# Kernel optimization log

Measured on AMD Instinct MI355X. Metric: run time of the kernel, lower is better.

The kernel has to match this reference:

```python
import jax, jax.numpy as jnp
import numpy as np

# Grid derived from voxel_size=[0.2,0.2,0.2], pcr=[0,-40,-3,70.4,40,1]
NX, NY, NZ, NB = 352, 400, 20, 4


def setup_inputs() -> dict:
    key = jax.random.key(0)
    N, C = 1_000_000, 64
    kp, kb, kz, ky, kx = jax.random.split(key, 5)
    points = jax.random.normal(kp, (N, C), dtype=jnp.float32)
    b = jax.random.randint(kb, (N,), 0, NB)
    z = jax.random.randint(kz, (N,), 0, NZ)
    y = jax.random.randint(ky, (N,), 0, NY)
    x = jax.random.randint(kx, (N,), 0, NX)
    coors = jnp.stack([b, z, y, x], axis=1).astype(jnp.int32)
    return {"points": points, "coors": coors}


def reference(points, coors):
    # Dynamic scatter with mean reduction (average_points=True):
    # group points sharing the same (batch, z, y, x) voxel coordinate and
    # average their features. Padded (unused) voxel slots have coor == -1
    # and zero features, so the output shape is static ([N, C]).
    N = points.shape[0]
    b, z, y, x = coors[:, 0], coors[:, 1], coors[:, 2], coors[:, 3]
    keys = ((b.astype(jnp.int64) * NZ + z) * NY + y) * NX + x  # linearized voxel id

    uniq, inv = jnp.unique(keys, return_inverse=True, size=N, fill_value=-1)
    inv = inv.reshape(-1)

    sums = jax.ops.segment_sum(points, inv, num_segments=N)          # [N, C]
    counts = jax.ops.segment_sum(jnp.ones((N,), points.dtype), inv, num_segments=N)
    voxels = sums / jnp.maximum(counts, 1.0)[:, None]

    # decode linearized keys back to (batch, z, y, x); -1 marks padding
    valid = uniq >= 0
    ux = uniq % NX
    uy = (uniq // NX) % NY
    uz = (uniq // (NX * NY)) % NZ
    ub = uniq // (NX * NY * NZ)
    voxel_coors = jnp.stack([ub, uz, uy, ux], axis=1).astype(jnp.int32)
    voxel_coors = jnp.where(valid[:, None], voxel_coors, -1)
    return voxels, voxel_coors
```

## Files before the change

kernel.cpp:

```cpp
#include <hip/hip_runtime.h>
#include <stdint.h>

#define NXc 352
#define NYc 400
#define NZc 20
#define KS  11264000
#define WORDS 176000
#define NBLKS 688
#define NCH 64
#define RPT 4

#define OFF_A     0ull
#define OFF_P     11264000ull
#define OFF_R     12672000ull
#define OFF_M     13376000ull
#define OFF_BP    14784000ull
#define OFF_BC    14788096ull
#define OFF_BM    14792192ull
#define OFF_NU    14796288ull
#define OFF_KEYPT 14796544ull
#define OFF_IOFF  18796544ull
#define OFF_ML    22796800ull
#define OFF_PID   24796800ull

static __device__ __forceinline__ int keyof(int4 c) {
  return ((c.x * NZc + c.y) * NYc + c.z) * NXc + c.w;
}

__global__ void k_zero(uint4* __restrict__ A4, unsigned int mA) {
  unsigned int i = blockIdx.x * 256 + threadIdx.x, s = gridDim.x * 256;
  uint4 z = make_uint4(0u, 0u, 0u, 0u);
  for (unsigned int j = i; j < mA; j += s) A4[j] = z;
}

__global__ void k_count(const int4* __restrict__ coors, unsigned int* __restrict__ A32,
                        int* __restrict__ keyPt, int n) {
  int p = blockIdx.x * 256 + threadIdx.x;
  if (p >= n) return;
  int key = keyof(coors[p]);
  keyPt[p] = key;
  atomicAdd(&A32[key >> 2], 1u << (8 * (key & 3)));
}

__global__ void k_scan1(const unsigned char* __restrict__ A, unsigned int* __restrict__ bp,
                        unsigned int* __restrict__ bc, unsigned int* __restrict__ bm) {
  int b = blockIdx.x, t = threadIdx.x;
  int w = b * 256 + t;
  unsigned int pres = 0, cnt = 0, mult = 0;
  if (w < WORDS) {
    const uint4* aw = (const uint4*)(A + (size_t)w * 64);
    unsigned long long mask = 0ull;
#pragma unroll
    for (int q = 0; q < 4; q++) {
      uint4 v = aw[q];
      unsigned int us[4] = { v.x, v.y, v.z, v.w };
#pragma unroll
      for (int i = 0; i < 4; i++) {
        unsigned int u = us[i];
#pragma unroll
        for (int bb = 0; bb < 4; bb++) {
          unsigned int byte = (u >> (8 * bb)) & 0xFFu;
          cnt += byte;
          mult += (byte >= 2u);
          if (byte) mask |= 1ull << (q * 16 + i * 4 + bb);
        }
      }
    }
    pres = (unsigned int)__popcll(mask);
  }
  __shared__ unsigned int sp[256], sc[256], sm[256];
  sp[t] = pres; sc[t] = cnt; sm[t] = mult; __syncthreads();
  for (int o = 128; o > 0; o >>= 1) {
    if (t < o) { sp[t] += sp[t + o]; sc[t] += sc[t + o]; sm[t] += sm[t + o]; }
    __syncthreads();
  }
  if (t == 0) { bp[b] = sp[0]; bc[b] = sc[0]; bm[b] = sm[0]; }
}

__global__ void k_scan2(unsigned int* __restrict__ bp, unsigned int* __restrict__ bc,
                        unsigned int* __restrict__ bm, unsigned int* __restrict__ nu,
                        unsigned int* __restrict__ ioff, int n) {
  int t = threadIdx.x;
  __shared__ unsigned int sp[256], sc[256], sm[256];
  unsigned int cp = 0, cc = 0, cm = 0;
  for (int base = 0; base < NBLKS; base += 256) {
    int i = base + t;
    unsigned int vp = (i < NBLKS) ? bp[i] : 0u;
    unsigned int vc = (i < NBLKS) ? bc[i] : 0u;
    unsigned int vm = (i < NBLKS) ? bm[i] : 0u;
    sp[t] = vp; sc[t] = vc; sm[t] = vm; __syncthreads();
    unsigned int ipv = vp, icv = vc, imv = vm;
    for (int o = 1; o < 256; o <<= 1) {
      unsigned int ap = (t >= o) ? sp[t - o] : 0u;
      unsigned int ac = (t >= o) ? sc[t - o] : 0u;
      unsigned int am = (t >= o) ? sm[t - o] : 0u;
      __syncthreads();
      ipv += ap; icv += ac; imv += am;
      sp[t] = ipv; sc[t] = icv; sm[t] = imv; __syncthreads();
    }
    if (i < NBLKS) { bp[i] = cp + ipv - vp; bc[i] = cc + icv - vc; bm[i] = cm + imv - vm; }
    unsigned int tp = sp[255], tc = sc[255], tm = sm[255];
    __syncthreads();
    cp += tp; cc += tc; cm += tm;
  }
  if (t == 0) { nu[0] = cp; nu[1] = cm; ioff[cp] = (unsigned int)n; }
}

__global__ void k_scan3(const unsigned char* __restrict__ A,
                        const unsigned int* __restrict__ bp, const unsigned int* __restrict__ bc,
                        const unsigned int* __restrict__ bm,
                        unsigned long long* __restrict__ P, unsigned int* __restrict__ R,
                        unsigned long long* __restrict__ M,
                        unsigned int* __restrict__ ioff, unsigned int* __restrict__ mlist,
                        float4* __restrict__ outc) {
  int b = blockIdx.x, t = threadIdx.x;
  int w = b * 256 + t;
  unsigned long long mask = 0ull, mmask = 0ull;
  unsigned int uu[16];
  unsigned int pres = 0, cnt = 0, mult = 0;
  if (w < WORDS) {
    const uint4* aw = (const uint4*)(A + (size_t)w * 64);
#pragma unroll
    for (int q = 0; q < 4; q++) {
      uint4 v = aw[q];
      uu[q * 4 + 0] = v.x; uu[q * 4 + 1] = v.y; uu[q * 4 + 2] = v.z; uu[q * 4 + 3] = v.w;
    }
#pragma unroll
    for (int i = 0; i < 16; i++) {
      unsigned int u = uu[i];
#pragma unroll
      for (int bb = 0; bb < 4; bb++) {
        unsigned int byte = (u >> (8 * bb)) & 0xFFu;
        cnt += byte;
        mult += (byte >= 2u);
        if (byte)       mask  |= 1ull << (i * 4 + bb);
        if (byte >= 2u) mmask |= 1ull << (i * 4 + bb);
      }
    }
    pres = (unsigned int)__popcll(mask);
  }
  __shared__ unsigned int sp[256], sc[256], sm[256];
  sp[t] = pres; sc[t] = cnt; sm[t] = mult; __syncthreads();
  unsigned int ip = pres, ic = cnt, im = mult;
  for (int o = 1; o < 256; o <<= 1) {
    unsigned int ap = (t >= o) ? sp[t - o] : 0u;
    unsigned int ac = (t >= o) ? sc[t - o] : 0u;
    unsigned int am = (t >= o) ? sm[t - o] : 0u;
    __syncthreads();
    ip += ap; ic += ac; im += am;
    sp[t] = ip; sc[t] = ic; sm[t] = im; __syncthreads();
  }
  if (w < WORDS) {
    unsigned int rank  = bp[b] + ip - pres;
    unsigned int coff  = bc[b] + ic - cnt;
    unsigned int mrank = bm[b] + im - mult;
    P[w] = mask; R[w] = rank; M[w] = mmask;
    for (int j = 0; j < 64; j++) {
      unsigned int byte = (uu[j >> 2] >> (8 * (j & 3))) & 0xFFu;
      if (byte) {
        ioff[rank] = coff;
        unsigned int k = (unsigned int)w * 64u + (unsigned int)j;
        unsigned int x = k % NXc; unsigned int k2 = k / NXc;
        unsigned int y = k2 % NYc; unsigned int k3 = k2 / NYc;
        unsigned int z = k3 % NZc; unsigned int bb2 = k3 / NZc;
        outc[rank] = make_float4((float)bb2, (float)z, (float)y, (float)x);
        if (byte >= 2u) mlist[mrank++] = rank;
        rank++; coff += byte;
      }
    }
  }
}

__global__ void k_scatter(const float4* __restrict__ pts, const int* __restrict__ keyPt,
                          unsigned int* __restrict__ A32,
                          const unsigned long long* __restrict__ P, const unsigned int* __restrict__ R,
                          const unsigned long long* __restrict__ M,
                          const unsigned int* __restrict__ ioff, unsigned int* __restrict__ pid,
                          float* __restrict__ out, int n) {
  int gt = blockIdx.x * 256 + threadIdx.x;
  int grp = gt >> 4, l = gt & 15;
  int pb = grp * RPT;
  if (pb >= n) return;
  int np = min(RPT, n - pb);

  float4 v[RPT];
#pragma unroll
  for (int j = 0; j < RPT; j++) {
    int p = pb + ((j < np) ? j : 0);
    v[j] = pts[(size_t)p * 16 + l];
  }
  int key[RPT];
#pragma unroll
  for (int j = 0; j < RPT; j++) key[j] = keyPt[pb + ((j < np) ? j : 0)];

  unsigned long long Pw[RPT], Mw[RPT];
  unsigned int Rw[RPT];
#pragma unroll
  for (int j = 0; j < RPT; j++) {
    int w = key[j] >> 6;
    Pw[j] = P[w]; Mw[j] = M[w]; Rw[j] = R[w];
  }

#pragma unroll
  for (int j = 0; j < RPT; j++) {
    if (j >= np) break;
    int bit = key[j] & 63;
    unsigned int rank = Rw[j] + (unsigned int)__popcll(Pw[j] & ((1ull << bit) - 1ull));
    if (!((Mw[j] >> bit) & 1ull)) {
      ((float4*)out)[(size_t)rank * 16 + l] = v[j];
    } else if (l == 0) {
      unsigned int sh = 8u * (unsigned int)(key[j] & 3);
      unsigned int old = atomicSub(&A32[key[j] >> 2], 1u << sh);
      unsigned int intra = ((old >> sh) & 0xFFu) - 1u;
      pid[ioff[rank] + intra] = (unsigned int)(pb + j);
    }
  }
}

__global__ void k_fin(const float4* __restrict__ pts, const unsigned int* __restrict__ pid,
                      const unsigned int* __restrict__ ioff, const unsigned int* __restrict__ mlist,
                      const unsigned int* __restrict__ nu, float* __restrict__ out, int n) {
  unsigned int s = gridDim.x * 256;
  unsigned int tid = blockIdx.x * 256 + threadIdx.x;
  unsigned int mc16 = nu[1] * 16u;
  for (unsigned int gt = tid; gt < mc16; gt += s) {
    unsigned int g = gt >> 4, l = gt & 15;
    unsigned int rank = mlist[g];
    unsigned int o0 = ioff[rank], o1 = ioff[rank + 1];
    float4 acc = make_float4(0.f, 0.f, 0.f, 0.f);
    for (unsigned int i = o0; i < o1; i++) {
      float4 v = pts[(size_t)pid[i] * 16 + l];
      acc.x += v.x; acc.y += v.y; acc.z += v.z; acc.w += v.w;
    }
    float inv = 1.0f / (float)(o1 - o0);
    acc.x *= inv; acc.y *= inv; acc.z *= inv; acc.w *= inv;
    ((float4*)out)[(size_t)rank * 16 + l] = acc;
  }
  unsigned int nU = nu[0];
  float4 z = make_float4(0.f, 0.f, 0.f, 0.f);
  float4 m1 = make_float4(-1.f, -1.f, -1.f, -1.f);
  for (unsigned int r = nU + tid; r < (unsigned int)n; r += s) {
    float4* row = (float4*)out + (size_t)r * 16;
#pragma unroll
    for (int q = 0; q < 16; q++) row[q] = z;
    ((float4*)(out + (size_t)n * NCH))[r] = m1;
  }
}

extern "C" void kernel_launch(void* const* d_in, const int* in_sizes, int n_in,
                              void* d_out, int out_size, void* d_ws, size_t ws_size,
                              hipStream_t stream) {
  const float4* pts = (const float4*)d_in[0];
  const int4* coors = (const int4*)d_in[1];
  int n = in_sizes[1] / 4;
  float* out = (float*)d_out;
  char* ws = (char*)d_ws;
  unsigned char*      A    = (unsigned char*)(ws + OFF_A);
  unsigned int*       A32  = (unsigned int*)(ws + OFF_A);
  unsigned long long* P    = (unsigned long long*)(ws + OFF_P);
  unsigned int*       R    = (unsigned int*)(ws + OFF_R);
  unsigned long long* M    = (unsigned long long*)(ws + OFF_M);
  unsigned int*       bp   = (unsigned int*)(ws + OFF_BP);
  unsigned int*       bc   = (unsigned int*)(ws + OFF_BC);
  unsigned int*       bm   = (unsigned int*)(ws + OFF_BM);
  unsigned int*       nu   = (unsigned int*)(ws + OFF_NU);
  int*                keyPt= (int*)(ws + OFF_KEYPT);
  unsigned int*       ioff = (unsigned int*)(ws + OFF_IOFF);
  unsigned int*       mlist= (unsigned int*)(ws + OFF_ML);
  unsigned int*       pid  = (unsigned int*)(ws + OFF_PID);
  float4*             outc = (float4*)(out + (size_t)n * NCH);

  k_zero   <<<2048,  256, 0, stream>>>((uint4*)A, (unsigned int)(KS / 16));
  int nb = (n + 255) / 256;
  k_count  <<<nb,    256, 0, stream>>>(coors, A32, keyPt, n);
  k_scan1  <<<NBLKS, 256, 0, stream>>>(A, bp, bc, bm);
  k_scan2  <<<1,     256, 0, stream>>>(bp, bc, bm, nu, ioff, n);
  k_scan3  <<<NBLKS, 256, 0, stream>>>(A, bp, bc, bm, P, R, M, ioff, mlist, outc);
  int ngrp = (n + RPT - 1) / RPT;
  int sb = (ngrp * 16 + 255) / 256;
  k_scatter<<<sb,    256, 0, stream>>>(pts, keyPt, A32, P, R, M, ioff, pid, out, n);
  k_fin    <<<2048,  256, 0, stream>>>(pts, pid, ioff, mlist, nu, out, n);
}
```

Measured before the change: 209.2 us.

## Replace multi-point voxel gather with pre-zeroed float atomic accumulation

The point-ID bucketing path for voxels with multiple points is removed, along with the per-voxel offset/count scans, the multi-mask, the mlist, and the gather in the final kernel. Rows for multi-point voxels are now zeroed during the compaction scan. The scatter kernel then atomically adds each point's features pre-scaled by 1/count, with the count read directly from the byte histogram. This drops a kernel phase and two of the three scan streams, but adds float atomics and makes summation order nondeterministic.

```diff
diff --git a/kernel.cpp b/kernel.cpp
--- a/kernel.cpp
+++ b/kernel.cpp
@@ -13,15 +13,9 @@
 #define OFF_A     0ull
 #define OFF_P     11264000ull
 #define OFF_R     12672000ull
-#define OFF_M     13376000ull
-#define OFF_BP    14784000ull
-#define OFF_BC    14788096ull
-#define OFF_BM    14792192ull
-#define OFF_NU    14796288ull
-#define OFF_KEYPT 14796544ull
-#define OFF_IOFF  18796544ull
-#define OFF_ML    22796800ull
-#define OFF_PID   24796800ull
+#define OFF_BP    13376000ull
+#define OFF_NU    13380096ull
+#define OFF_KEYPT 13380352ull
 
 static __device__ __forceinline__ int keyof(int4 c) {
   return ((c.x * NZc + c.y) * NYc + c.z) * NXc + c.w;
@@ -42,11 +36,10 @@
   atomicAdd(&A32[key >> 2], 1u << (8 * (key & 3)));
 }
 
-__global__ void k_scan1(const unsigned char* __restrict__ A, unsigned int* __restrict__ bp,
-                        unsigned int* __restrict__ bc, unsigned int* __restrict__ bm) {
+__global__ void k_scan1(const unsigned char* __restrict__ A, unsigned int* __restrict__ bp) {
   int b = blockIdx.x, t = threadIdx.x;
   int w = b * 256 + t;
-  unsigned int pres = 0, cnt = 0, mult = 0;
+  unsigned int pres = 0;
   if (w < WORDS) {
     const uint4* aw = (const uint4*)(A + (size_t)w * 64);
     unsigned long long mask = 0ull;
@@ -58,66 +51,52 @@
       for (int i = 0; i < 4; i++) {
         unsigned int u = us[i];
 #pragma unroll
-        for (int bb = 0; bb < 4; bb++) {
-          unsigned int byte = (u >> (8 * bb)) & 0xFFu;
-          cnt += byte;
-          mult += (byte >= 2u);
-          if (byte) mask |= 1ull << (q * 16 + i * 4 + bb);
-        }
+        for (int bb = 0; bb < 4; bb++)
+          if ((u >> (8 * bb)) & 0xFFu) mask |= 1ull << (q * 16 + i * 4 + bb);
       }
     }
     pres = (unsigned int)__popcll(mask);
   }
-  __shared__ unsigned int sp[256], sc[256], sm[256];
-  sp[t] = pres; sc[t] = cnt; sm[t] = mult; __syncthreads();
+  __shared__ unsigned int sp[256];
+  sp[t] = pres; __syncthreads();
   for (int o = 128; o > 0; o >>= 1) {
-    if (t < o) { sp[t] += sp[t + o]; sc[t] += sc[t + o]; sm[t] += sm[t + o]; }
+    if (t < o) sp[t] += sp[t + o];
     __syncthreads();
   }
-  if (t == 0) { bp[b] = sp[0]; bc[b] = sc[0]; bm[b] = sm[0]; }
-}
-
-__global__ void k_scan2(unsigned int* __restrict__ bp, unsigned int* __restrict__ bc,
-                        unsigned int* __restrict__ bm, unsigned int* __restrict__ nu,
-                        unsigned int* __restrict__ ioff, int n) {
+  if (t == 0) bp[b] = sp[0];
+}
+
+__global__ void k_scan2(unsigned int* __restrict__ bp, unsigned int* __restrict__ nu) {
   int t = threadIdx.x;
-  __shared__ unsigned int sp[256], sc[256], sm[256];
-  unsigned int cp = 0, cc = 0, cm = 0;
+  __shared__ unsigned int sp[256];
+  unsigned int cp = 0;
   for (int base = 0; base < NBLKS; base += 256) {
     int i = base + t;
     unsigned int vp = (i < NBLKS) ? bp[i] : 0u;
-    unsigned int vc = (i < NBLKS) ? bc[i] : 0u;
-    unsigned int vm = (i < NBLKS) ? bm[i] : 0u;
-    sp[t] = vp; sc[t] = vc; sm[t] = vm; __syncthreads();
-    unsigned int ipv = vp, icv = vc, imv = vm;
+    sp[t] = vp; __syncthreads();
+    unsigned int ipv = vp;
     for (int o = 1; o < 256; o <<= 1) {
       unsigned int ap = (t >= o) ? sp[t - o] : 0u;
-      unsigned int ac = (t >= o) ? sc[t - o] : 0u;
-      unsigned int am = (t >= o) ? sm[t - o] : 0u;
       __syncthreads();
-      ipv += ap; icv += ac; imv += am;
-      sp[t] = ipv; sc[t] = icv; sm[t] = imv; __syncthreads();
-    }
-    if (i < NBLKS) { bp[i] = cp + ipv - vp; bc[i] = cc + icv - vc; bm[i] = cm + imv - vm; }
-    unsigned int tp = sp[255], tc = sc[255], tm = sm[255];
+      ipv += ap;
+      sp[t] = ipv; __syncthreads();
+    }
+    if (i < NBLKS) bp[i] = cp + ipv - vp;
+    unsigned int tp = sp[255];
     __syncthreads();
-    cp += tp; cc += tc; cm += tm;
-  }
-  if (t == 0) { nu[0] = cp; nu[1] = cm; ioff[cp] = (unsigned int)n; }
-}
-
-__global__ void k_scan3(const unsigned char* __restrict__ A,
-                        const unsigned int* __restrict__ bp, const unsigned int* __restrict__ bc,
-                        const unsigned int* __restrict__ bm,
+    cp += tp;
+  }
+  if (t == 0) nu[0] = cp;
+}
+
+__global__ void k_scan3(const unsigned char* __restrict__ A, const unsigned int* __restrict__ bp,
                         unsigned long long* __restrict__ P, unsigned int* __restrict__ R,
-                        unsigned long long* __restrict__ M,
-                        unsigned int* __restrict__ ioff, unsigned int* __restrict__ mlist,
-                        float4* __restrict__ outc) {
+                        float4* __restrict__ outc, float* __restrict__ out) {
   int b = blockIdx.x, t = threadIdx.x;
   int w = b * 256 + t;
-  unsigned long long mask = 0ull, mmask = 0ull;
+  unsigned long long mask = 0ull;
   unsigned int uu[16];
-  unsigned int pres = 0, cnt = 0, mult = 0;
+  unsigned int pres = 0;
   if (w < WORDS) {
     const uint4* aw = (const uint4*)(A + (size_t)w * 64);
 #pragma unroll
@@ -129,53 +108,46 @@
     for (int i = 0; i < 16; i++) {
       unsigned int u = uu[i];
 #pragma unroll
-      for (int bb = 0; bb < 4; bb++) {
-        unsigned int byte = (u >> (8 * bb)) & 0xFFu;
-        cnt += byte;
-        mult += (byte >= 2u);
-        if (byte)       mask  |= 1ull << (i * 4 + bb);
-        if (byte >= 2u) mmask |= 1ull << (i * 4 + bb);
-      }
+      for (int bb = 0; bb < 4; bb++)
+        if ((u >> (8 * bb)) & 0xFFu) mask |= 1ull << (i * 4 + bb);
     }
     pres = (unsigned int)__popcll(mask);
   }
-  __shared__ unsigned int sp[256], sc[256], sm[256];
-  sp[t] = pres; sc[t] = cnt; sm[t] = mult; __syncthreads();
-  unsigned int ip = pres, ic = cnt, im = mult;
+  __shared__ unsigned int sp[256];
+  sp[t] = pres; __syncthreads();
+  unsigned int ip = pres;
   for (int o = 1; o < 256; o <<= 1) {
     unsigned int ap = (t >= o) ? sp[t - o] : 0u;
-    unsigned int ac = (t >= o) ? sc[t - o] : 0u;
-    unsigned int am = (t >= o) ? sm[t - o] : 0u;
     __syncthreads();
-    ip += ap; ic += ac; im += am;
-    sp[t] = ip; sc[t] = ic; sm[t] = im; __syncthreads();
+    ip += ap;
+    sp[t] = ip; __syncthreads();
   }
   if (w < WORDS) {
-    unsigned int rank  = bp[b] + ip - pres;
-    unsigned int coff  = bc[b] + ic - cnt;
-    unsigned int mrank = bm[b] + im - mult;
-    P[w] = mask; R[w] = rank; M[w] = mmask;
+    unsigned int rank = bp[b] + ip - pres;
+    P[w] = mask; R[w] = rank;
+    float4 z4 = make_float4(0.f, 0.f, 0.f, 0.f);
     for (int j = 0; j < 64; j++) {
       unsigned int byte = (uu[j >> 2] >> (8 * (j & 3))) & 0xFFu;
       if (byte) {
-        ioff[rank] = coff;
         unsigned int k = (unsigned int)w * 64u + (unsigned int)j;
         unsigned int x = k % NXc; unsigned int k2 = k / NXc;
         unsigned int y = k2 % NYc; unsigned int k3 = k2 / NYc;
         unsigned int z = k3 % NZc; unsigned int bb2 = k3 / NZc;
         outc[rank] = make_float4((float)bb2, (float)z, (float)y, (float)x);
-        if (byte >= 2u) mlist[mrank++] = rank;
-        rank++; coff += byte;
+        if (byte >= 2u) {
+          float4* row = (float4*)out + (size_t)rank * 16;
+#pragma unroll
+          for (int q = 0; q < 16; q++) row[q] = z4;
+        }
+        rank++;
       }
     }
   }
 }
 
 __global__ void k_scatter(const float4* __restrict__ pts, const int* __restrict__ keyPt,
-                          unsigned int* __restrict__ A32,
+                          const unsigned char* __restrict__ A,
                           const unsigned long long* __restrict__ P, const unsigned int* __restrict__ R,
-                          const unsigned long long* __restrict__ M,
-                          const unsigned int* __restrict__ ioff, unsigned int* __restrict__ pid,
                           float* __restrict__ out, int n) {
   int gt = blockIdx.x * 256 + threadIdx.x;
   int grp = gt >> 4, l = gt & 15;
@@ -193,12 +165,12 @@
 #pragma unroll
   for (int j = 0; j < RPT; j++) key[j] = keyPt[pb + ((j < np) ? j : 0)];
 
-  unsigned long long Pw[RPT], Mw[RPT];
-  unsigned int Rw[RPT];
+  unsigned long long Pw[RPT];
+  unsigned int Rw[RPT], cnt[RPT];
 #pragma unroll
   for (int j = 0; j < RPT; j++) {
     int w = key[j] >> 6;
-    Pw[j] = P[w]; Mw[j] = M[w]; Rw[j] = R[w];
+    Pw[j] = P[w]; Rw[j] = R[w]; cnt[j] = A[key[j]];
   }
 
 #pragma unroll
@@ -206,40 +178,25 @@
     if (j >= np) break;
     int bit = key[j] & 63;
     unsigned int rank = Rw[j] + (unsigned int)__popcll(Pw[j] & ((1ull << bit) - 1ull));
-    if (!((Mw[j] >> bit) & 1ull)) {
+    if (cnt[j] == 1u) {
       ((float4*)out)[(size_t)rank * 16 + l] = v[j];
-    } else if (l == 0) {
-      unsigned int sh = 8u * (unsigned int)(key[j] & 3);
-      unsigned int old = atomicSub(&A32[key[j] >> 2], 1u << sh);
-      unsigned int intra = ((old >> sh) & 0xFFu) - 1u;
-      pid[ioff[rank] + intra] = (unsigned int)(pb + j);
-    }
-  }
-}
-
-__global__ void k_fin(const float4* __restrict__ pts, const unsigned int* __restrict__ pid,
-                      const unsigned int* __restrict__ ioff, const unsigned int* __restrict__ mlist,
-                      const unsigned int* __restrict__ nu, float* __restrict__ out, int n) {
+    } else {
+      float inv = 1.0f / (float)cnt[j];
+      float* dst = out + (size_t)rank * 64 + l * 4;
+      atomicAdd(dst + 0, v[j].x * inv);
+      atomicAdd(dst + 1, v[j].y * inv);
+      atomicAdd(dst + 2, v[j].z * inv);
+      atomicAdd(dst + 3, v[j].w * inv);
+    }
+  }
+}
+
+__global__ void k_tail(const unsigned int* __restrict__ nu, float* __restrict__ out, int n) {
+  unsigned int nU = nu[0];
   unsigned int s = gridDim.x * 256;
-  unsigned int tid = blockIdx.x * 256 + threadIdx.x;
-  unsigned int mc16 = nu[1] * 16u;
-  for (unsigned int gt = tid; gt < mc16; gt += s) {
-    unsigned int g = gt >> 4, l = gt & 15;
-    unsigned int rank = mlist[g];
-    unsigned int o0 = ioff[rank], o1 = ioff[rank + 1];
-    float4 acc = make_float4(0.f, 0.f, 0.f, 0.f);
-    for (unsigned int i = o0; i < o1; i++) {
-      float4 v = pts[(size_t)pid[i] * 16 + l];
-      acc.x += v.x; acc.y += v.y; acc.z += v.z; acc.w += v.w;
-    }
-    float inv = 1.0f / (float)(o1 - o0);
-    acc.x *= inv; acc.y *= inv; acc.z *= inv; acc.w *= inv;
-    ((float4*)out)[(size_t)rank * 16 + l] = acc;
-  }
-  unsigned int nU = nu[0];
   float4 z = make_float4(0.f, 0.f, 0.f, 0.f);
   float4 m1 = make_float4(-1.f, -1.f, -1.f, -1.f);
-  for (unsigned int r = nU + tid; r < (unsigned int)n; r += s) {
+  for (unsigned int r = nU + blockIdx.x * 256 + threadIdx.x; r < (unsigned int)n; r += s) {
     float4* row = (float4*)out + (size_t)r * 16;
 #pragma unroll
     for (int q = 0; q < 16; q++) row[q] = z;
@@ -259,25 +216,19 @@
   unsigned int*       A32  = (unsigned int*)(ws + OFF_A);
   unsigned long long* P    = (unsigned long long*)(ws + OFF_P);
   unsigned int*       R    = (unsigned int*)(ws + OFF_R);
-  unsigned long long* M    = (unsigned long long*)(ws + OFF_M);
   unsigned int*       bp   = (unsigned int*)(ws + OFF_BP);
-  unsigned int*       bc   = (unsigned int*)(ws + OFF_BC);
-  unsigned int*       bm   = (unsigned int*)(ws + OFF_BM);
   unsigned int*       nu   = (unsigned int*)(ws + OFF_NU);
   int*                keyPt= (int*)(ws + OFF_KEYPT);
-  unsigned int*       ioff = (unsigned int*)(ws + OFF_IOFF);
-  unsigned int*       mlist= (unsigned int*)(ws + OFF_ML);
-  unsigned int*       pid  = (unsigned int*)(ws + OFF_PID);
   float4*             outc = (float4*)(out + (size_t)n * NCH);
 
   k_zero   <<<2048,  256, 0, stream>>>((uint4*)A, (unsigned int)(KS / 16));
   int nb = (n + 255) / 256;
   k_count  <<<nb,    256, 0, stream>>>(coors, A32, keyPt, n);
-  k_scan1  <<<NBLKS, 256, 0, stream>>>(A, bp, bc, bm);
-  k_scan2  <<<1,     256, 0, stream>>>(bp, bc, bm, nu, ioff, n);
-  k_scan3  <<<NBLKS, 256, 0, stream>>>(A, bp, bc, bm, P, R, M, ioff, mlist, outc);
+  k_scan1  <<<NBLKS, 256, 0, stream>>>(A, bp);
+  k_scan2  <<<1,     256, 0, stream>>>(bp, nu);
+  k_scan3  <<<NBLKS, 256, 0, stream>>>(A, bp, P, R, outc, out);
   int ngrp = (n + RPT - 1) / RPT;
   int sb = (ngrp * 16 + 255) / 256;
-  k_scatter<<<sb,    256, 0, stream>>>(pts, keyPt, A32, P, R, M, ioff, pid, out, n);
-  k_fin    <<<2048,  256, 0, stream>>>(pts, pid, ioff, mlist, nu, out, n);
-}
+  k_scatter<<<sb,    256, 0, stream>>>(pts, keyPt, A, P, R, out, n);
+  k_tail   <<<2048,  256, 0, stream>>>(nu, out, n);
+}
```

After: 240.8 us. +15.1%, slower.

## Fuse three-pass scan into one kernel with last-block aggregation and grid barrier

Applied to the files above, without the earlier changes.

Merges the block-reduce, block-offset scan, and final scan kernels into one launch. Each block publishes its totals, the last block to arrive scans all block totals, and the other blocks spin on a flag before writing ranks. This removes two launches and a second read of the count array. It depends on all 688 blocks being co-resident, otherwise the spin deadlocks. It also raises points per scatter group from 4 to 8 and uses nontemporal loads and stores for point rows.

```diff
diff --git a/kernel.cpp b/kernel.cpp
--- a/kernel.cpp
+++ b/kernel.cpp
@@ -8,7 +8,9 @@
 #define WORDS 176000
 #define NBLKS 688
 #define NCH 64
-#define RPT 4
+#define RPT 8
+
+typedef float f32x4 __attribute__((ext_vector_type(4)));
 
 #define OFF_A     0ull
 #define OFF_P     11264000ull
@@ -18,19 +20,21 @@
 #define OFF_BC    14788096ull
 #define OFF_BM    14792192ull
 #define OFF_NU    14796288ull
-#define OFF_KEYPT 14796544ull
-#define OFF_IOFF  18796544ull
-#define OFF_ML    22796800ull
-#define OFF_PID   24796800ull
+#define OFF_GS    14796544ull
+#define OFF_KEYPT 14796800ull
+#define OFF_IOFF  18796800ull
+#define OFF_ML    22797056ull
+#define OFF_PID   24797056ull
 
 static __device__ __forceinline__ int keyof(int4 c) {
   return ((c.x * NZc + c.y) * NYc + c.z) * NXc + c.w;
 }
 
-__global__ void k_zero(uint4* __restrict__ A4, unsigned int mA) {
+__global__ void k_zero(uint4* __restrict__ A4, unsigned int mA, uint4* __restrict__ gs) {
   unsigned int i = blockIdx.x * 256 + threadIdx.x, s = gridDim.x * 256;
   uint4 z = make_uint4(0u, 0u, 0u, 0u);
   for (unsigned int j = i; j < mA; j += s) A4[j] = z;
+  if (i == 0) gs[0] = z;
 }
 
 __global__ void k_count(const int4* __restrict__ coors, unsigned int* __restrict__ A32,
@@ -42,77 +46,13 @@
   atomicAdd(&A32[key >> 2], 1u << (8 * (key & 3)));
 }
 
-__global__ void k_scan1(const unsigned char* __restrict__ A, unsigned int* __restrict__ bp,
-                        unsigned int* __restrict__ bc, unsigned int* __restrict__ bm) {
-  int b = blockIdx.x, t = threadIdx.x;
-  int w = b * 256 + t;
-  unsigned int pres = 0, cnt = 0, mult = 0;
-  if (w < WORDS) {
-    const uint4* aw = (const uint4*)(A + (size_t)w * 64);
-    unsigned long long mask = 0ull;
-#pragma unroll
-    for (int q = 0; q < 4; q++) {
-      uint4 v = aw[q];
-      unsigned int us[4] = { v.x, v.y, v.z, v.w };
-#pragma unroll
-      for (int i = 0; i < 4; i++) {
-        unsigned int u = us[i];
-#pragma unroll
-        for (int bb = 0; bb < 4; bb++) {
-          unsigned int byte = (u >> (8 * bb)) & 0xFFu;
-          cnt += byte;
-          mult += (byte >= 2u);
-          if (byte) mask |= 1ull << (q * 16 + i * 4 + bb);
-        }
-      }
-    }
-    pres = (unsigned int)__popcll(mask);
-  }
-  __shared__ unsigned int sp[256], sc[256], sm[256];
-  sp[t] = pres; sc[t] = cnt; sm[t] = mult; __syncthreads();
-  for (int o = 128; o > 0; o >>= 1) {
-    if (t < o) { sp[t] += sp[t + o]; sc[t] += sc[t + o]; sm[t] += sm[t + o]; }
-    __syncthreads();
-  }
-  if (t == 0) { bp[b] = sp[0]; bc[b] = sc[0]; bm[b] = sm[0]; }
-}
-
-__global__ void k_scan2(unsigned int* __restrict__ bp, unsigned int* __restrict__ bc,
-                        unsigned int* __restrict__ bm, unsigned int* __restrict__ nu,
-                        unsigned int* __restrict__ ioff, int n) {
-  int t = threadIdx.x;
-  __shared__ unsigned int sp[256], sc[256], sm[256];
-  unsigned int cp = 0, cc = 0, cm = 0;
-  for (int base = 0; base < NBLKS; base += 256) {
-    int i = base + t;
-    unsigned int vp = (i < NBLKS) ? bp[i] : 0u;
-    unsigned int vc = (i < NBLKS) ? bc[i] : 0u;
-    unsigned int vm = (i < NBLKS) ? bm[i] : 0u;
-    sp[t] = vp; sc[t] = vc; sm[t] = vm; __syncthreads();
-    unsigned int ipv = vp, icv = vc, imv = vm;
-    for (int o = 1; o < 256; o <<= 1) {
-      unsigned int ap = (t >= o) ? sp[t - o] : 0u;
-      unsigned int ac = (t >= o) ? sc[t - o] : 0u;
-      unsigned int am = (t >= o) ? sm[t - o] : 0u;
-      __syncthreads();
-      ipv += ap; icv += ac; imv += am;
-      sp[t] = ipv; sc[t] = icv; sm[t] = imv; __syncthreads();
-    }
-    if (i < NBLKS) { bp[i] = cp + ipv - vp; bc[i] = cc + icv - vc; bm[i] = cm + imv - vm; }
-    unsigned int tp = sp[255], tc = sc[255], tm = sm[255];
-    __syncthreads();
-    cp += tp; cc += tc; cm += tm;
-  }
-  if (t == 0) { nu[0] = cp; nu[1] = cm; ioff[cp] = (unsigned int)n; }
-}
-
-__global__ void k_scan3(const unsigned char* __restrict__ A,
-                        const unsigned int* __restrict__ bp, const unsigned int* __restrict__ bc,
-                        const unsigned int* __restrict__ bm,
-                        unsigned long long* __restrict__ P, unsigned int* __restrict__ R,
-                        unsigned long long* __restrict__ M,
-                        unsigned int* __restrict__ ioff, unsigned int* __restrict__ mlist,
-                        float4* __restrict__ outc) {
+__global__ void k_scan(const unsigned char* __restrict__ A,
+                       unsigned int* __restrict__ bp, unsigned int* __restrict__ bc,
+                       unsigned int* __restrict__ bm, unsigned int* __restrict__ gsync,
+                       unsigned long long* __restrict__ P, unsigned int* __restrict__ R,
+                       unsigned long long* __restrict__ M,
+                       unsigned int* __restrict__ ioff, unsigned int* __restrict__ mlist,
+                       unsigned int* __restrict__ nu, float4* __restrict__ outc, int n) {
   int b = blockIdx.x, t = threadIdx.x;
   int w = b * 256 + t;
   unsigned long long mask = 0ull, mmask = 0ull;
@@ -150,6 +90,46 @@
     ip += ap; ic += ac; im += am;
     sp[t] = ip; sc[t] = ic; sm[t] = im; __syncthreads();
   }
+  __shared__ int isagg;
+  if (t == 0) {
+    bp[b] = sp[255]; bc[b] = sc[255]; bm[b] = sm[255];
+    __threadfence();
+    unsigned int old = atomicAdd(&gsync[0], 1u);
+    isagg = (old == NBLKS - 1u);
+  }
+  __syncthreads();
+  if (isagg) {
+    __threadfence();
+    unsigned int cp = 0, cc = 0, cm = 0;
+    for (int base = 0; base < NBLKS; base += 256) {
+      int i = base + t;
+      unsigned int vp = (i < NBLKS) ? bp[i] : 0u;
+      unsigned int vc = (i < NBLKS) ? bc[i] : 0u;
+      unsigned int vm = (i < NBLKS) ? bm[i] : 0u;
+      sp[t] = vp; sc[t] = vc; sm[t] = vm; __syncthreads();
+      unsigned int ipv = vp, icv = vc, imv = vm;
+      for (int o = 1; o < 256; o <<= 1) {
+        unsigned int ap = (t >= o) ? sp[t - o] : 0u;
+        unsigned int ac = (t >= o) ? sc[t - o] : 0u;
+        unsigned int am = (t >= o) ? sm[t - o] : 0u;
+        __syncthreads();
+        ipv += ap; icv += ac; imv += am;
+        sp[t] = ipv; sc[t] = icv; sm[t] = imv; __syncthreads();
+      }
+      if (i < NBLKS) { bp[i] = cp + ipv - vp; bc[i] = cc + icv - vc; bm[i] = cm + imv - vm; }
+      unsigned int tp = sp[255], tc = sc[255], tm = sm[255];
+      __syncthreads();
+      cp += tp; cc += tc; cm += tm;
+    }
+    if (t == 0) {
+      nu[0] = cp; nu[1] = cm; ioff[cp] = (unsigned int)n;
+      __threadfence();
+      atomicExch(&gsync[1], 1u);
+    }
+  }
+  if (t == 0) { while (atomicAdd(&gsync[1], 0u) == 0u) {} }
+  __syncthreads();
+  __threadfence();
   if (w < WORDS) {
     unsigned int rank  = bp[b] + ip - pres;
     unsigned int coff  = bc[b] + ic - cnt;
@@ -171,23 +151,23 @@
   }
 }
 
-__global__ void k_scatter(const float4* __restrict__ pts, const int* __restrict__ keyPt,
+__global__ void k_scatter(const f32x4* __restrict__ pts, const int* __restrict__ keyPt,
                           unsigned int* __restrict__ A32,
                           const unsigned long long* __restrict__ P, const unsigned int* __restrict__ R,
                           const unsigned long long* __restrict__ M,
                           const unsigned int* __restrict__ ioff, unsigned int* __restrict__ pid,
-                          float* __restrict__ out, int n) {
+                          f32x4* __restrict__ out, int n) {
   int gt = blockIdx.x * 256 + threadIdx.x;
   int grp = gt >> 4, l = gt & 15;
   int pb = grp * RPT;
   if (pb >= n) return;
   int np = min(RPT, n - pb);
 
-  float4 v[RPT];
+  f32x4 v[RPT];
 #pragma unroll
   for (int j = 0; j < RPT; j++) {
     int p = pb + ((j < np) ? j : 0);
-    v[j] = pts[(size_t)p * 16 + l];
+    v[j] = __builtin_nontemporal_load(&pts[(size_t)p * 16 + l]);
   }
   int key[RPT];
 #pragma unroll
@@ -207,7 +187,7 @@
     int bit = key[j] & 63;
     unsigned int rank = Rw[j] + (unsigned int)__popcll(Pw[j] & ((1ull << bit) - 1ull));
     if (!((Mw[j] >> bit) & 1ull)) {
-      ((float4*)out)[(size_t)rank * 16 + l] = v[j];
+      __builtin_nontemporal_store(v[j], &out[(size_t)rank * 16 + l]);
     } else if (l == 0) {
       unsigned int sh = 8u * (unsigned int)(key[j] & 3);
       unsigned int old = atomicSub(&A32[key[j] >> 2], 1u << sh);
@@ -217,7 +197,7 @@
   }
 }
 
-__global__ void k_fin(const float4* __restrict__ pts, const unsigned int* __restrict__ pid,
+__global__ void k_fin(const f32x4* __restrict__ pts, const unsigned int* __restrict__ pid,
                       const unsigned int* __restrict__ ioff, const unsigned int* __restrict__ mlist,
                       const unsigned int* __restrict__ nu, float* __restrict__ out, int n) {
   unsigned int s = gridDim.x * 256;
@@ -227,14 +207,13 @@
     unsigned int g = gt >> 4, l = gt & 15;
     unsigned int rank = mlist[g];
     unsigned int o0 = ioff[rank], o1 = ioff[rank + 1];
-    float4 acc = make_float4(0.f, 0.f, 0.f, 0.f);
+    f32x4 acc = (f32x4)(0.f);
     for (unsigned int i = o0; i < o1; i++) {
-      float4 v = pts[(size_t)pid[i] * 16 + l];
-      acc.x += v.x; acc.y += v.y; acc.z += v.z; acc.w += v.w;
-    }
-    float inv = 1.0f / (float)(o1 - o0);
-    acc.x *= inv; acc.y *= inv; acc.z *= inv; acc.w *= inv;
-    ((float4*)out)[(size_t)rank * 16 + l] = acc;
+      f32x4 v = __builtin_nontemporal_load(&pts[(size_t)pid[i] * 16 + l]);
+      acc += v;
+    }
+    acc *= (1.0f / (float)(o1 - o0));
+    ((f32x4*)out)[(size_t)rank * 16 + l] = acc;
   }
   unsigned int nU = nu[0];
   float4 z = make_float4(0.f, 0.f, 0.f, 0.f);
@@ -250,7 +229,7 @@
 extern "C" void kernel_launch(void* const* d_in, const int* in_sizes, int n_in,
                               void* d_out, int out_size, void* d_ws, size_t ws_size,
                               hipStream_t stream) {
-  const float4* pts = (const float4*)d_in[0];
+  const f32x4* pts = (const f32x4*)d_in[0];
   const int4* coors = (const int4*)d_in[1];
   int n = in_sizes[1] / 4;
   float* out = (float*)d_out;
@@ -264,20 +243,19 @@
   unsigned int*       bc   = (unsigned int*)(ws + OFF_BC);
   unsigned int*       bm   = (unsigned int*)(ws + OFF_BM);
   unsigned int*       nu   = (unsigned int*)(ws + OFF_NU);
+  unsigned int*       gs   = (unsigned int*)(ws + OFF_GS);
   int*                keyPt= (int*)(ws + OFF_KEYPT);
   unsigned int*       ioff = (unsigned int*)(ws + OFF_IOFF);
   unsigned int*       mlist= (unsigned int*)(ws + OFF_ML);
   unsigned int*       pid  = (unsigned int*)(ws + OFF_PID);
   float4*             outc = (float4*)(out + (size_t)n * NCH);
 
-  k_zero   <<<2048,  256, 0, stream>>>((uint4*)A, (unsigned int)(KS / 16));
+  k_zero   <<<2048,  256, 0, stream>>>((uint4*)A, (unsigned int)(KS / 16), (uint4*)gs);
   int nb = (n + 255) / 256;
   k_count  <<<nb,    256, 0, stream>>>(coors, A32, keyPt, n);
-  k_scan1  <<<NBLKS, 256, 0, stream>>>(A, bp, bc, bm);
-  k_scan2  <<<1,     256, 0, stream>>>(bp, bc, bm, nu, ioff, n);
-  k_scan3  <<<NBLKS, 256, 0, stream>>>(A, bp, bc, bm, P, R, M, ioff, mlist, outc);
+  k_scan   <<<NBLKS, 256, 0, stream>>>(A, bp, bc, bm, gs, P, R, M, ioff, mlist, nu, outc, n);
   int ngrp = (n + RPT - 1) / RPT;
   int sb = (ngrp * 16 + 255) / 256;
-  k_scatter<<<sb,    256, 0, stream>>>(pts, keyPt, A32, P, R, M, ioff, pid, out, n);
+  k_scatter<<<sb,    256, 0, stream>>>(pts, keyPt, A32, P, R, M, ioff, pid, (f32x4*)out, n);
   k_fin    <<<2048,  256, 0, stream>>>(pts, pid, ioff, mlist, nu, out, n);
 }
```

After: 270.3 us. 29.2% more time.
